# Kernel tuning notes

Hardware: AMD Instinct MI355X
Metric: run time of the kernel (lower is better)

The kernel has to match this reference:

```python
import jax, jax.numpy as jnp
import numpy as np

DIM = 1024
HEADS = 8
DIM_HEAD = 64
DIM_INNER = HEADS * DIM_HEAD  # 512


def setup_inputs() -> dict:
    key = jax.random.key(0)
    k1, k2, k3, k4 = jax.random.split(key, 4)
    x = jax.random.normal(k1, (1, 4096, DIM), dtype=jnp.float32)
    gamma = jnp.ones((DIM,), dtype=jnp.float32)
    w_qkv = jax.random.normal(k2, (DIM, 3 * DIM_INNER), dtype=jnp.float32) * (DIM ** -0.5)
    w_out = jax.random.normal(k3, (DIM_INNER, DIM), dtype=jnp.float32) * (DIM_INNER ** -0.5)
    return {"x": x, "gamma": gamma, "w_qkv": w_qkv, "w_out": w_out}


def _rmsnorm(x, gamma):
    # F.normalize(x, dim=-1) * sqrt(dim) * gamma
    norm = jnp.sqrt(jnp.sum(x * x, axis=-1, keepdims=True))
    x = x / jnp.maximum(norm, 1e-12)
    return x * (DIM ** 0.5) * gamma


def reference(x, gamma, w_qkv, w_out):
    b, n, _ = x.shape
    h, d = HEADS, DIM_HEAD
    normed = _rmsnorm(x, gamma)
    qkv = normed @ w_qkv  # [b, n, 3*h*d]
    qkv = qkv.reshape(b, n, 3, h, d)
    q = jnp.transpose(qkv[:, :, 0], (0, 2, 1, 3))  # b h n d
    k = jnp.transpose(qkv[:, :, 1], (0, 2, 1, 3))
    v = jnp.transpose(qkv[:, :, 2], (0, 2, 1, 3))
    # default_attention (faithful: scales q by d**0.5 as in source)
    q = q * (d ** 0.5)
    sim = jnp.einsum('bhid,bhjd->bhij', q, k)
    mask_value = -jnp.finfo(sim.dtype).max
    causal_mask = jnp.triu(jnp.ones((n, n), dtype=bool), 1)
    sim = jnp.where(causal_mask, mask_value, sim)
    attn = jax.nn.softmax(sim, axis=-1)
    out = jnp.einsum('bhij,bhjd->bhid', attn, v)  # b h n d
    out = jnp.transpose(out, (0, 2, 1, 3)).reshape(b, n, h * d)
    return out @ w_out  # [b, n, dim]
```

## Files before the change

kernel.cpp:

```cpp
#include <hip/hip_runtime.h>
#include <math.h>

#define SEQ 4096
#define DIM 1024
#define HEADS 8
#define DINNER 512
#define QKVW 1536
#define PAD 80

typedef unsigned short u16;
typedef __attribute__((ext_vector_type(8))) short s8v;
typedef __attribute__((ext_vector_type(4))) float f4v;
#define MFMA(a, b, c) __builtin_amdgcn_mfma_f32_16x16x32_bf16(a, b, c, 0, 0, 0)

__device__ __forceinline__ u16 f2bf(float f) {
    unsigned u = __float_as_uint(f);
    u += 0x7fff + ((u >> 16) & 1);
    return (u16)(u >> 16);
}
__device__ __forceinline__ float bf2f(u16 b) { return __uint_as_float(((unsigned)b) << 16); }

__global__ __launch_bounds__(256) void rmsnorm_split(const float* __restrict__ x,
                                                     const float* __restrict__ gamma,
                                                     u16* __restrict__ hi,
                                                     u16* __restrict__ lo) {
    __shared__ float red[4];
    const int row = blockIdx.x, t = threadIdx.x;
    const float* xr = x + (size_t)row * DIM;
    float v[4];
    float ss = 0.f;
#pragma unroll
    for (int i = 0; i < 4; ++i) { v[i] = xr[t + i * 256]; ss += v[i] * v[i]; }
#pragma unroll
    for (int off = 32; off >= 1; off >>= 1) ss += __shfl_xor(ss, off, 64);
    if ((t & 63) == 0) red[t >> 6] = ss;
    __syncthreads();
    float scale = 32.0f / fmaxf(sqrtf(red[0] + red[1] + red[2] + red[3]), 1e-12f);
#pragma unroll
    for (int i = 0; i < 4; ++i) {
        int c = t + i * 256;
        float y = v[i] * scale * gamma[c];
        u16 h = f2bf(y);
        hi[(size_t)row * DIM + c] = h;
        lo[(size_t)row * DIM + c] = f2bf(y - bf2f(h));
    }
}

__global__ __launch_bounds__(256) void transpose_split(const float* __restrict__ in,
                                                       u16* __restrict__ hi,
                                                       u16* __restrict__ lo,
                                                       int R, int C, int want_lo) {
    __shared__ float tile[64][65];
    const int c0 = blockIdx.x * 64, r0 = blockIdx.y * 64;
    const int t = threadIdx.x, col = t & 63, rb = t >> 6;
#pragma unroll
    for (int j = 0; j < 16; ++j)
        tile[rb + j * 4][col] = in[(size_t)(r0 + rb + j * 4) * C + c0 + col];
    __syncthreads();
#pragma unroll
    for (int j = 0; j < 16; ++j) {
        int cc = rb + j * 4;
        float v = tile[col][cc];
        size_t oi = (size_t)(c0 + cc) * R + r0 + col;
        u16 h = f2bf(v);
        hi[oi] = h;
        if (want_lo) lo[oi] = f2bf(v - bf2f(h));
    }
}

__global__ __launch_bounds__(256) void gemm_qkv_split(
    const u16* __restrict__ Ah, const u16* __restrict__ Al,
    const u16* __restrict__ Bh, const u16* __restrict__ Bl,
    u16* __restrict__ qh, u16* __restrict__ ql,
    u16* __restrict__ kh, u16* __restrict__ kl, u16* __restrict__ vtp) {
    __shared__ u16 Ash[64 * PAD], Asl[64 * PAD], Bsh[64 * PAD], Bsl[64 * PAD];
    const int t = threadIdx.x;
    const int bn = blockIdx.x * 64, bm = blockIdx.y * 64;
    const int w = t >> 6, lane = t & 63, m = lane & 15, q = lane >> 4;
    f4v acc[4] = {{0.f, 0.f, 0.f, 0.f}, {0.f, 0.f, 0.f, 0.f},
                  {0.f, 0.f, 0.f, 0.f}, {0.f, 0.f, 0.f, 0.f}};
    for (int k0 = 0; k0 < DIM; k0 += 64) {
        __syncthreads();
#pragma unroll
        for (int i = 0; i < 2; ++i) {
            int c = t + i * 256, row = c >> 3, ch = (c & 7) * 8;
            *(uint4*)&Ash[row * PAD + ch] = *(const uint4*)&Ah[(size_t)(bm + row) * DIM + k0 + ch];
            *(uint4*)&Asl[row * PAD + ch] = *(const uint4*)&Al[(size_t)(bm + row) * DIM + k0 + ch];
            *(uint4*)&Bsh[row * PAD + ch] = *(const uint4*)&Bh[(size_t)(bn + row) * DIM + k0 + ch];
            *(uint4*)&Bsl[row * PAD + ch] = *(const uint4*)&Bl[(size_t)(bn + row) * DIM + k0 + ch];
        }
        __syncthreads();
#pragma unroll
        for (int kk = 0; kk < 64; kk += 32) {
            s8v ah = *(const s8v*)&Ash[(w * 16 + m) * PAD + kk + q * 8];
            s8v al = *(const s8v*)&Asl[(w * 16 + m) * PAD + kk + q * 8];
#pragma unroll
            for (int ct = 0; ct < 4; ++ct) {
                s8v bh = *(const s8v*)&Bsh[(ct * 16 + m) * PAD + kk + q * 8];
                s8v bl = *(const s8v*)&Bsl[(ct * 16 + m) * PAD + kk + q * 8];
                acc[ct] = MFMA(ah, bh, acc[ct]);
                acc[ct] = MFMA(al, bh, acc[ct]);
                acc[ct] = MFMA(ah, bl, acc[ct]);
            }
        }
    }
    const int region = bn >> 9;
#pragma unroll
    for (int ct = 0; ct < 4; ++ct) {
#pragma unroll
        for (int r = 0; r < 4; ++r) {
            int gr = bm + w * 16 + q * 4 + r;
            int gc = bn + ct * 16 + m;
            float v = acc[ct][r];
            if (region == 0) {
                v *= 8.0f;
                u16 h = f2bf(v);
                qh[(size_t)gr * DINNER + gc] = h;
                ql[(size_t)gr * DINNER + gc] = f2bf(v - bf2f(h));
            } else if (region == 1) {
                u16 h = f2bf(v);
                kh[(size_t)gr * DINNER + (gc - 512)] = h;
                kl[(size_t)gr * DINNER + (gc - 512)] = f2bf(v - bf2f(h));
            } else {
                vtp[(size_t)(gc - 1024) * SEQ + gr] = f2bf(v);
            }
        }
    }
}

__global__ __launch_bounds__(256) void attn_mfma(
    const u16* __restrict__ qh, const u16* __restrict__ ql,
    const u16* __restrict__ kh, const u16* __restrict__ kl,
    const u16* __restrict__ vt, u16* __restrict__ atto) {
    __shared__ u16 Qh[64 * PAD], Ql[64 * PAD], KP[64 * PAD], Kl[64 * PAD], Vt[64 * PAD];
    const int t = threadIdx.x;
    const int qt = blockIdx.x, h = blockIdx.y;
    const int w = t >> 6, lane = t & 63, m = lane & 15, q = lane >> 4;

#pragma unroll
    for (int i = 0; i < 2; ++i) {
        int c = t + i * 256, row = c >> 3, ch = (c & 7) * 8;
        *(uint4*)&Qh[row * PAD + ch] =
            *(const uint4*)&qh[(size_t)(qt * 64 + row) * DINNER + h * 64 + ch];
        *(uint4*)&Ql[row * PAD + ch] =
            *(const uint4*)&ql[(size_t)(qt * 64 + row) * DINNER + h * 64 + ch];
    }

    f4v o[4] = {{0.f, 0.f, 0.f, 0.f}, {0.f, 0.f, 0.f, 0.f},
                {0.f, 0.f, 0.f, 0.f}, {0.f, 0.f, 0.f, 0.f}};
    float mi[4] = {-1e30f, -1e30f, -1e30f, -1e30f};
    float li[4] = {0.f, 0.f, 0.f, 0.f};

    for (int kt = 0; kt <= qt; ++kt) {
        __syncthreads();
#pragma unroll
        for (int i = 0; i < 2; ++i) {
            int c = t + i * 256, row = c >> 3, ch = (c & 7) * 8;
            *(uint4*)&KP[row * PAD + ch] =
                *(const uint4*)&kh[(size_t)(kt * 64 + row) * DINNER + h * 64 + ch];
            *(uint4*)&Kl[row * PAD + ch] =
                *(const uint4*)&kl[(size_t)(kt * 64 + row) * DINNER + h * 64 + ch];
            *(uint4*)&Vt[row * PAD + ch] =
                *(const uint4*)&vt[(size_t)(h * 64 + row) * SEQ + kt * 64 + ch];
        }
        __syncthreads();

        f4v s[4] = {{0.f, 0.f, 0.f, 0.f}, {0.f, 0.f, 0.f, 0.f},
                    {0.f, 0.f, 0.f, 0.f}, {0.f, 0.f, 0.f, 0.f}};
#pragma unroll
        for (int kk = 0; kk < 64; kk += 32) {
            s8v ah = *(const s8v*)&Qh[(w * 16 + m) * PAD + kk + q * 8];
            s8v al = *(const s8v*)&Ql[(w * 16 + m) * PAD + kk + q * 8];
#pragma unroll
            for (int ct = 0; ct < 4; ++ct) {
                s8v bh = *(const s8v*)&KP[(ct * 16 + m) * PAD + kk + q * 8];
                s8v bl = *(const s8v*)&Kl[(ct * 16 + m) * PAD + kk + q * 8];
                s[ct] = MFMA(ah, bh, s[ct]);
                s[ct] = MFMA(al, bh, s[ct]);
                s[ct] = MFMA(ah, bl, s[ct]);
            }
        }
        if (kt == qt) {
#pragma unroll
            for (int ct = 0; ct < 4; ++ct)
#pragma unroll
                for (int r = 0; r < 4; ++r)
                    if (ct * 16 + m > w * 16 + q * 4 + r) s[ct][r] = -1e30f;
        }

        float alpha[4];
#pragma unroll
        for (int r = 0; r < 4; ++r) {
            float rm = fmaxf(fmaxf(s[0][r], s[1][r]), fmaxf(s[2][r], s[3][r]));
#pragma unroll
            for (int off = 8; off >= 1; off >>= 1) rm = fmaxf(rm, __shfl_xor(rm, off, 64));
            float mn = fmaxf(mi[r], rm);
            alpha[r] = __expf(mi[r] - mn);
            mi[r] = mn;
            float rs = 0.f;
#pragma unroll
            for (int ct = 0; ct < 4; ++ct) {
                s[ct][r] = __expf(s[ct][r] - mn);
                rs += s[ct][r];
            }
#pragma unroll
            for (int off = 8; off >= 1; off >>= 1) rs += __shfl_xor(rs, off, 64);
            li[r] = li[r] * alpha[r] + rs;
        }

        __syncthreads();
#pragma unroll
        for (int ct = 0; ct < 4; ++ct)
#pragma unroll
            for (int r = 0; r < 4; ++r) {
                KP[(w * 16 + q * 4 + r) * PAD + ct * 16 + m] = f2bf(s[ct][r]);
                o[ct][r] *= alpha[r];
            }
#pragma unroll
        for (int kk = 0; kk < 64; kk += 32) {
            s8v ap = *(const s8v*)&KP[(w * 16 + m) * PAD + kk + q * 8];
#pragma unroll
            for (int ct = 0; ct < 4; ++ct) {
                s8v bv = *(const s8v*)&Vt[(ct * 16 + m) * PAD + kk + q * 8];
                o[ct] = MFMA(ap, bv, o[ct]);
            }
        }
    }

#pragma unroll
    for (int r = 0; r < 4; ++r) {
        float inv = 1.0f / li[r];
#pragma unroll
        for (int ct = 0; ct < 4; ++ct)
            atto[(size_t)(qt * 64 + w * 16 + q * 4 + r) * DINNER + h * 64 + ct * 16 + m] =
                f2bf(o[ct][r] * inv);
    }
}

__global__ __launch_bounds__(256) void gemm_out_bf16(const u16* __restrict__ A,
                                                     const u16* __restrict__ Bt,
                                                     float* __restrict__ C) {
    __shared__ u16 As[64 * PAD], Bs[64 * PAD];
    const int t = threadIdx.x;
    const int bn = blockIdx.x * 64, bm = blockIdx.y * 64;
    const int w = t >> 6, lane = t & 63, m = lane & 15, q = lane >> 4;
    f4v acc[4] = {{0.f, 0.f, 0.f, 0.f}, {0.f, 0.f, 0.f, 0.f},
                  {0.f, 0.f, 0.f, 0.f}, {0.f, 0.f, 0.f, 0.f}};
    for (int k0 = 0; k0 < DINNER; k0 += 64) {
        __syncthreads();
#pragma unroll
        for (int i = 0; i < 2; ++i) {
            int c = t + i * 256, row = c >> 3, ch = (c & 7) * 8;
            *(uint4*)&As[row * PAD + ch] = *(const uint4*)&A[(size_t)(bm + row) * DINNER + k0 + ch];
            *(uint4*)&Bs[row * PAD + ch] = *(const uint4*)&Bt[(size_t)(bn + row) * DINNER + k0 + ch];
        }
        __syncthreads();
#pragma unroll
        for (int kk = 0; kk < 64; kk += 32) {
            s8v a = *(const s8v*)&As[(w * 16 + m) * PAD + kk + q * 8];
#pragma unroll
            for (int ct = 0; ct < 4; ++ct) {
                s8v b = *(const s8v*)&Bs[(ct * 16 + m) * PAD + kk + q * 8];
                acc[ct] = MFMA(a, b, acc[ct]);
            }
        }
    }
#pragma unroll
    for (int ct = 0; ct < 4; ++ct)
#pragma unroll
        for (int r = 0; r < 4; ++r)
            C[(size_t)(bm + w * 16 + q * 4 + r) * DIM + bn + ct * 16 + m] = acc[ct][r];
}

extern "C" void kernel_launch(void* const* d_in, const int* in_sizes, int n_in,
                              void* d_out, int out_size, void* d_ws, size_t ws_size,
                              hipStream_t stream) {
    const float* x     = (const float*)d_in[0];
    const float* gamma = (const float*)d_in[1];
    const float* w_qkv = (const float*)d_in[2];
    const float* w_out = (const float*)d_in[3];
    float* out = (float*)d_out;

    u16* nh = (u16*)d_out;
    u16* nl = nh + (size_t)SEQ * DIM;

    u16* p = (u16*)d_ws;
    u16* wqt_h = p; p += (size_t)QKVW * DIM;
    u16* wqt_l = p; p += (size_t)QKVW * DIM;
    u16* wot   = p; p += (size_t)DIM * DINNER;
    u16* qh = p; p += (size_t)SEQ * DINNER;
    u16* ql = p; p += (size_t)SEQ * DINNER;
    u16* kh = p; p += (size_t)SEQ * DINNER;
    u16* kl = p; p += (size_t)SEQ * DINNER;
    u16* vt = p; p += (size_t)DINNER * SEQ;
    u16* atto = p; p += (size_t)SEQ * DINNER;

    transpose_split<<<dim3(QKVW / 64, DIM / 64), 256, 0, stream>>>(w_qkv, wqt_h, wqt_l,
                                                                   DIM, QKVW, 1);
    transpose_split<<<dim3(DIM / 64, DINNER / 64), 256, 0, stream>>>(w_out, wot, nullptr,
                                                                     DINNER, DIM, 0);
    rmsnorm_split<<<SEQ, 256, 0, stream>>>(x, gamma, nh, nl);
    gemm_qkv_split<<<dim3(QKVW / 64, SEQ / 64), 256, 0, stream>>>(nh, nl, wqt_h, wqt_l,
                                                                  qh, ql, kh, kl, vt);
    attn_mfma<<<dim3(SEQ / 64, HEADS), 256, 0, stream>>>(qh, ql, kh, kl, vt, atto);
    gemm_out_bf16<<<dim3(DIM / 64, SEQ / 64), 256, 0, stream>>>(atto, wot, out);
}
```

Measured before the change: 295.4 us.

## Split causal attention over key chunks with register prefetch and merge kernel

Splits the attention over the KV sequence into four chunks of 16 tiles (flash-decoding style). Each chunk writes an unnormalized partial output plus running max and sum, and a new merge kernel combines the chunks. This removes the long tail from the causal triangle, where late query tiles walked every key tile, and gives more blocks to fill the GPU. It also prefetches the next K/V tile into registers during compute, and moves P into its own LDS buffer so one barrier can be dropped. In exchange it adds partial-result traffic (stored in bf16 in the output buffer), an extra launch, and more LDS per block.

```diff
diff --git a/kernel.cpp b/kernel.cpp
--- a/kernel.cpp
+++ b/kernel.cpp
@@ -7,6 +7,8 @@
 #define DINNER 512
 #define QKVW 1536
 #define PAD 80
+#define NCHUNK 4
+#define CHUNK_KT 16
 
 typedef unsigned short u16;
 typedef __attribute__((ext_vector_type(8))) short s8v;
@@ -128,18 +130,23 @@
     }
 }
 
-__global__ __launch_bounds__(256) void attn_mfma(
+__global__ __launch_bounds__(256) void attn_part(
     const u16* __restrict__ qh, const u16* __restrict__ ql,
     const u16* __restrict__ kh, const u16* __restrict__ kl,
-    const u16* __restrict__ vt, u16* __restrict__ atto) {
-    __shared__ u16 Qh[64 * PAD], Ql[64 * PAD], KP[64 * PAD], Kl[64 * PAD], Vt[64 * PAD];
+    const u16* __restrict__ vt, u16* __restrict__ po,
+    float* __restrict__ pm, float* __restrict__ pl) {
+    __shared__ u16 Qh[64 * PAD], Ql[64 * PAD], Kh[64 * PAD], Kl[64 * PAD],
+                   Vt[64 * PAD], Ps[64 * PAD];
+    const int qt = blockIdx.x, h = blockIdx.y, c = blockIdx.z;
+    if (qt < c * CHUNK_KT) return;
     const int t = threadIdx.x;
-    const int qt = blockIdx.x, h = blockIdx.y;
     const int w = t >> 6, lane = t & 63, m = lane & 15, q = lane >> 4;
+    const int kbeg = c * CHUNK_KT;
+    const int kend = min(c * CHUNK_KT + CHUNK_KT, qt + 1);
 
 #pragma unroll
     for (int i = 0; i < 2; ++i) {
-        int c = t + i * 256, row = c >> 3, ch = (c & 7) * 8;
+        int cc = t + i * 256, row = cc >> 3, ch = (cc & 7) * 8;
         *(uint4*)&Qh[row * PAD + ch] =
             *(const uint4*)&qh[(size_t)(qt * 64 + row) * DINNER + h * 64 + ch];
         *(uint4*)&Ql[row * PAD + ch] =
@@ -151,19 +158,34 @@
     float mi[4] = {-1e30f, -1e30f, -1e30f, -1e30f};
     float li[4] = {0.f, 0.f, 0.f, 0.f};
 
-    for (int kt = 0; kt <= qt; ++kt) {
-        __syncthreads();
-#pragma unroll
-        for (int i = 0; i < 2; ++i) {
-            int c = t + i * 256, row = c >> 3, ch = (c & 7) * 8;
-            *(uint4*)&KP[row * PAD + ch] =
-                *(const uint4*)&kh[(size_t)(kt * 64 + row) * DINNER + h * 64 + ch];
-            *(uint4*)&Kl[row * PAD + ch] =
-                *(const uint4*)&kl[(size_t)(kt * 64 + row) * DINNER + h * 64 + ch];
-            *(uint4*)&Vt[row * PAD + ch] =
-                *(const uint4*)&vt[(size_t)(h * 64 + row) * SEQ + kt * 64 + ch];
-        }
-        __syncthreads();
+    uint4 rkh[2], rkl[2], rv[2];
+    const int cc0 = t, cc1 = t + 256;
+    const int prow0 = cc0 >> 3, pch0 = (cc0 & 7) * 8;
+    const int prow1 = cc1 >> 3, pch1 = (cc1 & 7) * 8;
+
+#define ISSUE(kt_)                                                                       \
+    do {                                                                                 \
+        rkh[0] = *(const uint4*)&kh[(size_t)((kt_)*64 + prow0) * DINNER + h * 64 + pch0];\
+        rkh[1] = *(const uint4*)&kh[(size_t)((kt_)*64 + prow1) * DINNER + h * 64 + pch1];\
+        rkl[0] = *(const uint4*)&kl[(size_t)((kt_)*64 + prow0) * DINNER + h * 64 + pch0];\
+        rkl[1] = *(const uint4*)&kl[(size_t)((kt_)*64 + prow1) * DINNER + h * 64 + pch1];\
+        rv[0]  = *(const uint4*)&vt[(size_t)(h * 64 + prow0) * SEQ + (kt_)*64 + pch0];   \
+        rv[1]  = *(const uint4*)&vt[(size_t)(h * 64 + prow1) * SEQ + (kt_)*64 + pch1];   \
+    } while (0)
+
+    ISSUE(kbeg);
+
+    for (int kt = kbeg; kt < kend; ++kt) {
+        __syncthreads();
+        *(uint4*)&Kh[prow0 * PAD + pch0] = rkh[0];
+        *(uint4*)&Kh[prow1 * PAD + pch1] = rkh[1];
+        *(uint4*)&Kl[prow0 * PAD + pch0] = rkl[0];
+        *(uint4*)&Kl[prow1 * PAD + pch1] = rkl[1];
+        *(uint4*)&Vt[prow0 * PAD + pch0] = rv[0];
+        *(uint4*)&Vt[prow1 * PAD + pch1] = rv[1];
+        __syncthreads();
+        int ktn = (kt + 1 < kend) ? kt + 1 : kt;
+        ISSUE(ktn);
 
         f4v s[4] = {{0.f, 0.f, 0.f, 0.f}, {0.f, 0.f, 0.f, 0.f},
                     {0.f, 0.f, 0.f, 0.f}, {0.f, 0.f, 0.f, 0.f}};
@@ -173,7 +195,7 @@
             s8v al = *(const s8v*)&Ql[(w * 16 + m) * PAD + kk + q * 8];
 #pragma unroll
             for (int ct = 0; ct < 4; ++ct) {
-                s8v bh = *(const s8v*)&KP[(ct * 16 + m) * PAD + kk + q * 8];
+                s8v bh = *(const s8v*)&Kh[(ct * 16 + m) * PAD + kk + q * 8];
                 s8v bl = *(const s8v*)&Kl[(ct * 16 + m) * PAD + kk + q * 8];
                 s[ct] = MFMA(ah, bh, s[ct]);
                 s[ct] = MFMA(al, bh, s[ct]);
@@ -208,17 +230,16 @@
             li[r] = li[r] * alpha[r] + rs;
         }
 
-        __syncthreads();
 #pragma unroll
         for (int ct = 0; ct < 4; ++ct)
 #pragma unroll
             for (int r = 0; r < 4; ++r) {
-                KP[(w * 16 + q * 4 + r) * PAD + ct * 16 + m] = f2bf(s[ct][r]);
+                Ps[(w * 16 + q * 4 + r) * PAD + ct * 16 + m] = f2bf(s[ct][r]);
                 o[ct][r] *= alpha[r];
             }
 #pragma unroll
         for (int kk = 0; kk < 64; kk += 32) {
-            s8v ap = *(const s8v*)&KP[(w * 16 + m) * PAD + kk + q * 8];
+            s8v ap = *(const s8v*)&Ps[(w * 16 + m) * PAD + kk + q * 8];
 #pragma unroll
             for (int ct = 0; ct < 4; ++ct) {
                 s8v bv = *(const s8v*)&Vt[(ct * 16 + m) * PAD + kk + q * 8];
@@ -226,15 +247,38 @@
             }
         }
     }
+#undef ISSUE
 
 #pragma unroll
     for (int r = 0; r < 4; ++r) {
-        float inv = 1.0f / li[r];
+        int grow = qt * 64 + w * 16 + q * 4 + r;
+        size_t base = ((size_t)(c * HEADS + h) * SEQ + grow);
 #pragma unroll
         for (int ct = 0; ct < 4; ++ct)
-            atto[(size_t)(qt * 64 + w * 16 + q * 4 + r) * DINNER + h * 64 + ct * 16 + m] =
-                f2bf(o[ct][r] * inv);
-    }
+            po[base * 64 + ct * 16 + m] = f2bf(o[ct][r]);
+        if (m == 0) { pm[base] = mi[r]; pl[base] = li[r]; }
+    }
+}
+
+__global__ __launch_bounds__(256) void attn_merge(const u16* __restrict__ po,
+                                                  const float* __restrict__ pm,
+                                                  const float* __restrict__ pl,
+                                                  u16* __restrict__ atto) {
+    const int h = blockIdx.y;
+    const int row = blockIdx.x * 4 + (threadIdx.x >> 6);
+    const int d = threadIdx.x & 63;
+    const int nc = (row >> 10) + 1;
+    float M = -1e30f;
+    for (int c = 0; c < nc; ++c)
+        M = fmaxf(M, pm[(size_t)(c * HEADS + h) * SEQ + row]);
+    float L = 0.f, O = 0.f;
+    for (int c = 0; c < nc; ++c) {
+        size_t base = (size_t)(c * HEADS + h) * SEQ + row;
+        float e = __expf(pm[base] - M);
+        L += pl[base] * e;
+        O += bf2f(po[base * 64 + d]) * e;
+    }
+    atto[(size_t)row * DINNER + h * 64 + d] = f2bf(O / L);
 }
 
 __global__ __launch_bounds__(256) void gemm_out_bf16(const u16* __restrict__ A,
@@ -283,6 +327,7 @@
 
     u16* nh = (u16*)d_out;
     u16* nl = nh + (size_t)SEQ * DIM;
+    u16* po = (u16*)d_out;
 
     u16* p = (u16*)d_ws;
     u16* wqt_h = p; p += (size_t)QKVW * DIM;
@@ -294,6 +339,8 @@
     u16* kl = p; p += (size_t)SEQ * DINNER;
     u16* vt = p; p += (size_t)DINNER * SEQ;
     u16* atto = p; p += (size_t)SEQ * DINNER;
+    float* pm = (float*)p; p += (size_t)2 * NCHUNK * HEADS * SEQ;
+    float* pl = (float*)p; p += (size_t)2 * NCHUNK * HEADS * SEQ;
 
     transpose_split<<<dim3(QKVW / 64, DIM / 64), 256, 0, stream>>>(w_qkv, wqt_h, wqt_l,
                                                                    DIM, QKVW, 1);
@@ -302,6 +349,8 @@
     rmsnorm_split<<<SEQ, 256, 0, stream>>>(x, gamma, nh, nl);
     gemm_qkv_split<<<dim3(QKVW / 64, SEQ / 64), 256, 0, stream>>>(nh, nl, wqt_h, wqt_l,
                                                                   qh, ql, kh, kl, vt);
-    attn_mfma<<<dim3(SEQ / 64, HEADS), 256, 0, stream>>>(qh, ql, kh, kl, vt, atto);
+    attn_part<<<dim3(SEQ / 64, HEADS, NCHUNK), 256, 0, stream>>>(qh, ql, kh, kl, vt,
+                                                                 po, pm, pl);
+    attn_merge<<<dim3(SEQ / 4, HEADS), 256, 0, stream>>>(po, pm, pl, atto);
     gemm_out_bf16<<<dim3(DIM / 64, SEQ / 64), 256, 0, stream>>>(atto, wot, out);
 }
```

Result: no change. 300.8 us (+1.8%).
